# Performance work log

Measured on AMD Instinct MI355X. Metric: run time of the kernel, lower is better.

The kernel has to match this reference:

```python
import jax, jax.numpy as jnp
import numpy as np

N_E = 1024
E_DIM = 256
BETA = 0.25


def setup_inputs() -> dict:
    key = jax.random.key(0)
    k1, k2 = jax.random.split(key)
    z = jax.random.normal(k1, (16, 256, 64, 64), dtype=jnp.float32)
    # embedding initialized uniform(-1/n_e, 1/n_e)
    emb = jax.random.uniform(k2, (N_E, E_DIM), dtype=jnp.float32,
                             minval=-1.0 / N_E, maxval=1.0 / N_E)
    return {"z": z, "emb": emb}


def reference(z, emb):
    # z: [B, C, H, W] with C == e_dim; emb: [n_e, e_dim]
    z_perm = jnp.transpose(z, (0, 2, 3, 1))            # [B, H, W, C]
    zf = z_perm.reshape(-1, E_DIM)                      # [N, C]

    # pairwise squared distances: ||z||^2 + ||e||^2 - 2 z e^T  -> [N, n_e]
    d = (jnp.sum(zf * zf, axis=1, keepdims=True)
         + jnp.sum(emb * emb, axis=1)
         - 2.0 * jnp.matmul(zf, emb.T))

    idx = jnp.argmin(d, axis=1)                         # [N]
    zq_flat = emb[idx]                                  # gather [N, C]
    z_q = zq_flat.reshape(z_perm.shape)                 # [B, H, W, C]

    one_hot = jax.nn.one_hot(idx, N_E, dtype=jnp.float32)  # [N, n_e]

    codebook_loss = jnp.mean((jax.lax.stop_gradient(z_q) - z_perm) ** 2)
    commitment_loss = jnp.mean((z_q - jax.lax.stop_gradient(z_perm)) ** 2)
    loss = codebook_loss + BETA * commitment_loss

    # straight-through estimator
    z_q = z_perm + jax.lax.stop_gradient(z_q - z_perm)

    e_mean = jnp.mean(one_hot, axis=0)                  # [n_e]
    perplexity = jnp.exp(-jnp.sum(e_mean * jnp.log(e_mean + 1e-10)))

    z_q = jnp.transpose(z_q, (0, 3, 1, 2))              # [B, C, H, W]
    idx_ret = idx[:, None]
    return (z_q, loss, perplexity, one_hot, idx_ret, d)
```

## Files before the change

### kernel.cpp

```cpp
#include <hip/hip_runtime.h>
#include <math.h>


typedef unsigned short ushort;
typedef unsigned int uint;
typedef __attribute__((ext_vector_type(8))) short  bf16x8;
typedef __attribute__((ext_vector_type(8))) ushort ushort8v;
typedef __attribute__((ext_vector_type(4))) float  f32x4;

static const size_t O_LOSS = 16777216;
static const size_t O_PERP = 16777217;
static const size_t O_OH   = 16777218;
static const size_t O_IDX  = 83886082;
static const size_t O_D    = 83951618;

static const size_t WS_ENORM = 0;
static const size_t WS_ZNF   = 4096;
static const size_t WS_IDX   = 266240;
static const size_t WS_HIST  = 528384;
static const size_t WS_FCNT  = 532480;
static const size_t WS_FROWS = 532496;
static const size_t WS_LOSS  = 794640;
static const size_t WS_TOP2  = 802832;
static const size_t WS_AHI   = 9191440;
static const size_t WS_BHI   = 42745872;

#define THR_FLAG 4e-4f

__device__ __forceinline__ ushort f2bf(float f) {
  uint u = __float_as_uint(f);
  return (ushort)((u + 0x7FFFu + ((u >> 16) & 1u)) >> 16);
}
__device__ __forceinline__ void gload16(const void* g, void* l) {
  __builtin_amdgcn_global_load_lds(
      (const __attribute__((address_space(1))) void*)g,
      (__attribute__((address_space(3))) void*)l, 16, 0, 0);
}

__global__ __launch_bounds__(256) void vq_prep_e(const float* __restrict__ emb,
    float* __restrict__ enormf, ushort* __restrict__ Bhi,
    int* __restrict__ hist, int* __restrict__ flag_cnt) {
  const int j = blockIdx.x * 256 + threadIdx.x;
  hist[j] = 0;
  if (j == 0) *flag_cnt = 0;
  const float* e = emb + ((size_t)j << 8);
  ushort* br = Bhi + ((size_t)j << 8);
  double s = 0.0;
  for (int k0 = 0; k0 < 256; k0 += 8) {
    const float4 a = *(const float4*)&e[k0];
    const float4 b = *(const float4*)&e[k0 + 4];
    ushort8v v;
    v[0] = f2bf(a.x); v[1] = f2bf(a.y); v[2] = f2bf(a.z); v[3] = f2bf(a.w);
    v[4] = f2bf(b.x); v[5] = f2bf(b.y); v[6] = f2bf(b.z); v[7] = f2bf(b.w);
    *(ushort8v*)&br[k0] = v;
    s += (double)a.x * (double)a.x;  s += (double)a.y * (double)a.y;
    s += (double)a.z * (double)a.z;  s += (double)a.w * (double)a.w;
    s += (double)b.x * (double)b.x;  s += (double)b.y * (double)b.y;
    s += (double)b.z * (double)b.z;  s += (double)b.w * (double)b.w;
  }
  enormf[j] = (float)s;
}

__global__ __launch_bounds__(256) void vq_prep_z(const float* __restrict__ z,
    ushort* __restrict__ Ahi, float* __restrict__ znf) {
  __shared__ float As[256][68];
  __shared__ double znp[64][4];
  const int t = threadIdx.x;
  const int lane = t & 63, quad = t >> 6;
  const int blk = blockIdx.x;
  const float* zb = z + (((size_t)(blk >> 6)) << 20) + (((size_t)(blk & 63)) << 6);
  {
    const int kr = t >> 4, xc = (t & 15) << 2;
    for (int k0 = 0; k0 < 256; k0 += 16) {
      const int k = k0 + kr;
      *(float4*)&As[k][xc] = *(const float4*)&zb[((size_t)k << 12) + xc];
    }
  }
  __syncthreads();
  {
    double s = 0.0;
    const int kb = quad << 6;
    for (int k = 0; k < 64; ++k) { const double v = (double)As[kb + k][lane]; s += v * v; }
    znp[lane][quad] = s;
  }
  __syncthreads();
  const int m0 = ((blk >> 6) << 12) + ((blk & 63) << 6);
  if (t < 64) znf[m0 + t] = (float)(znp[t][0] + znp[t][1] + znp[t][2] + znp[t][3]);
  const int row = t >> 2;
  ushort* dst = Ahi + ((size_t)(m0 + row) << 8);
  for (int s = 0; s < 8; ++s) {
    const int k0 = ((t & 3) + (s << 2)) << 3;
    ushort8v v;
#pragma unroll
    for (int i = 0; i < 8; ++i) v[i] = f2bf(As[k0 + i][row]);
    *(ushort8v*)&dst[k0] = v;
  }
}

__global__ __launch_bounds__(256) void vq_gemm(const ushort* __restrict__ Ahi,
    const ushort* __restrict__ Bhi, const float* __restrict__ znf,
    const float* __restrict__ enormf, float* __restrict__ dmat,
    float4* __restrict__ top2) {
  __shared__ ushort As[16384];
  __shared__ ushort Bs[16384];

  const int t = threadIdx.x;
  const int lane = t & 63;
  const int w = t >> 6;
  const int wr = w >> 1, wc = w & 1;
  const int g = lane >> 4, cl = lane & 15;
  const int m0 = blockIdx.x << 7;
  const int n0 = blockIdx.y << 7;

  f32x4 acc[4][4];
#pragma unroll
  for (int a = 0; a < 4; ++a)
#pragma unroll
    for (int b = 0; b < 4; ++b) acc[a][b] = (f32x4)(0.0f);

  const int s0 = t, s1 = 256 + t;
  const int rA0 = s0 >> 2, cA0 = (s0 & 3) << 3;
  const int rA1 = s1 >> 2, cA1 = (s1 & 3) << 3;

#pragma unroll
  for (int p = 0; p < 2; ++p) {
    const int kb = p << 7;
    __syncthreads();
#pragma unroll
    for (int c = 0; c < 4; ++c) {
      const int koff = kb + (c << 5);
      gload16(Ahi + ((size_t)(m0 + rA0) << 8) + koff + cA0, &As[(c << 12) + (s0 << 3)]);
      gload16(Ahi + ((size_t)(m0 + rA1) << 8) + koff + cA1, &As[(c << 12) + (s1 << 3)]);
      gload16(Bhi + ((size_t)(n0 + rA0) << 8) + koff + cA0, &Bs[(c << 12) + (s0 << 3)]);
      gload16(Bhi + ((size_t)(n0 + rA1) << 8) + koff + cA1, &Bs[(c << 12) + (s1 << 3)]);
    }
    __syncthreads();
#pragma unroll
    for (int c2 = 0; c2 < 4; ++c2) {
      bf16x8 av[4], bv[4];
#pragma unroll
      for (int ai = 0; ai < 4; ++ai)
        av[ai] = *(const bf16x8*)&As[(c2 << 12) + ((wr << 6) + (ai << 4) + cl) * 32 + (g << 3)];
#pragma unroll
      for (int bj = 0; bj < 4; ++bj)
        bv[bj] = *(const bf16x8*)&Bs[(c2 << 12) + ((wc << 6) + (bj << 4) + cl) * 32 + (g << 3)];
#pragma unroll
      for (int ai = 0; ai < 4; ++ai)
#pragma unroll
        for (int bj = 0; bj < 4; ++bj)
          acc[ai][bj] = __builtin_amdgcn_mfma_f32_16x16x32_bf16(av[ai], bv[bj], acc[ai][bj], 0, 0, 0);
    }
  }

  __syncthreads();
  float* sd1 = (float*)As;
  int*   si1 = (int*)(sd1 + 256);
  float* sd2 = (float*)(si1 + 256);

  float zn_[4][4];
#pragma unroll
  for (int ai = 0; ai < 4; ++ai)
#pragma unroll
    for (int rg = 0; rg < 4; ++rg)
      zn_[ai][rg] = znf[m0 + (wr << 6) + (ai << 4) + (g << 2) + rg];
  float en_[4];
#pragma unroll
  for (int bj = 0; bj < 4; ++bj)
    en_[bj] = enormf[n0 + (wc << 6) + (bj << 4) + cl];

#pragma unroll
  for (int ai = 0; ai < 4; ++ai) {
#pragma unroll
    for (int rg = 0; rg < 4; ++rg) {
      const int m = m0 + (wr << 6) + (ai << 4) + (g << 2) + rg;
      const float zr = zn_[ai][rg];
      float m1 = 3.0e38f, m2 = 3.0e38f; int i1 = 0;
#pragma unroll
      for (int bj = 0; bj < 4; ++bj) {
        const float S = zr + en_[bj];
        const float v = S - 2.0f * acc[ai][bj][rg];
        const int n = n0 + (wc << 6) + (bj << 4) + cl;
        dmat[((size_t)m << 10) + n] = v;
        if (v < m1) { m2 = m1; m1 = v; i1 = n; }
        else if (v < m2) { m2 = v; }
      }
#pragma unroll
      for (int off = 8; off >= 1; off >>= 1) {
        const float o1 = __shfl_xor(m1, off, 16);
        const int   oi = __shfl_xor(i1, off, 16);
        const float o2 = __shfl_xor(m2, off, 16);
        const float ns = fminf(fminf(m2, o2), fmaxf(m1, o1));
        if (o1 < m1 || (o1 == m1 && oi < i1)) { m1 = o1; i1 = oi; }
        m2 = ns;
      }
      if (cl == 0) {
        const int r = (wr << 6) + (ai << 4) + (g << 2) + rg;
        sd1[(r << 1) + wc] = m1; si1[(r << 1) + wc] = i1; sd2[(r << 1) + wc] = m2;
      }
    }
  }
  __syncthreads();
  if (t < 128) {
    const float a1 = sd1[t << 1], b1 = sd1[(t << 1) + 1];
    const int ai1 = si1[t << 1], bi1 = si1[(t << 1) + 1];
    const float a2 = sd2[t << 1], b2 = sd2[(t << 1) + 1];
    float d1, d2; int i1;
    if (b1 < a1 || (b1 == a1 && bi1 < ai1)) { d1 = b1; i1 = bi1; d2 = fminf(a1, b2); }
    else { d1 = a1; i1 = ai1; d2 = fminf(b1, a2); }
    float4 r; r.x = d1; r.y = __int_as_float(i1); r.z = d2; r.w = 0.0f;
    top2[(((size_t)(m0 + t)) << 3) + blockIdx.y] = r;
  }
}

__global__ __launch_bounds__(256) void vq_top2merge(const float4* __restrict__ top2,
    int* __restrict__ idxw, int* __restrict__ flag_cnt, int* __restrict__ flag_rows,
    double* __restrict__ loss_part) {
  __shared__ double red[256];
  const int t = threadIdx.x;
  const int row = blockIdx.x * 256 + t;
  const float4* tp = top2 + ((size_t)row << 3);
  float4 e = tp[0];
  float d1 = e.x; int i1 = __float_as_int(e.y); float d2 = e.z;
  for (int k = 1; k < 8; ++k) {
    e = tp[k];
    const int ei = __float_as_int(e.y);
    if (e.x < d1 || (e.x == d1 && ei < i1)) { d2 = fminf(d1, e.z); d1 = e.x; i1 = ei; }
    else { d2 = fminf(d2, fminf(e.x, e.z)); }
  }
  idxw[row] = i1;
  if (d2 - d1 < THR_FLAG) {
    const int p = atomicAdd(flag_cnt, 1);
    flag_rows[p] = row;
  }
  red[t] = (double)d1;
  __syncthreads();
  for (int off = 128; off > 0; off >>= 1) {
    if (t < off) red[t] += red[t + off];
    __syncthreads();
  }
  if (t == 0) loss_part[blockIdx.x] = red[0];
}

__global__ __launch_bounds__(256) void vq_refine(const float* __restrict__ z,
    const float* __restrict__ emb, const float* __restrict__ znf,
    const float* __restrict__ enormf, const float* __restrict__ dmat,
    const int* __restrict__ flag_cnt, const int* __restrict__ flag_rows,
    int* __restrict__ idxw) {
  __shared__ float zrow[256];
  __shared__ float dmin_s[4];
  __shared__ int cand[256];
  __shared__ int ncand_s;
  __shared__ float rv[256];
  __shared__ int ri[256];
  const int t = threadIdx.x;
  const int n = *flag_cnt;
  for (int f = blockIdx.x; f < n; f += gridDim.x) {
    const int m = flag_rows[f];
    __syncthreads();
    if (t == 0) ncand_s = 0;
    zrow[t] = z[(((size_t)(m >> 12)) << 20) + (size_t)(m & 4095) + ((size_t)t << 12)];
    const float* dr = dmat + ((size_t)m << 10);
    const float2 a = *(const float2*)&dr[t << 2];
    const float2 b = *(const float2*)&dr[(t << 2) + 2];
    float dmin = fminf(fminf(a.x, a.y), fminf(b.x, b.y));
    for (int off = 32; off >= 1; off >>= 1) dmin = fminf(dmin, __shfl_xor(dmin, off));
    if ((t & 63) == 0) dmin_s[t >> 6] = dmin;
    __syncthreads();
    dmin = fminf(fminf(dmin_s[0], dmin_s[1]), fminf(dmin_s[2], dmin_s[3]));
    const float lim = dmin + THR_FLAG;
    const float dv[4] = {a.x, a.y, b.x, b.y};
#pragma unroll
    for (int q = 0; q < 4; ++q)
      if (dv[q] <= lim) {
        const int p = atomicAdd(&ncand_s, 1);
        if (p < 256) cand[p] = (t << 2) + q;
      }
    __syncthreads();
    const int nc = min(ncand_s, 256);
    float best = 3.0e38f; int bi = 1 << 30;
    if (t < nc) {
      const int j = cand[t];
      const float* er = emb + ((size_t)j << 8);
      float s = 0.0f;
      for (int k = 0; k < 256; ++k) s = fmaf(zrow[k], er[k], s);
      const float S = znf[m] + enormf[j];
      best = S - 2.0f * s;
      bi = j;
    }
    rv[t] = best; ri[t] = bi;
    __syncthreads();
    for (int off = 128; off > 0; off >>= 1) {
      if (t < off) {
        const float ov = rv[t + off]; const int oi = ri[t + off];
        if (ov < rv[t] || (ov == rv[t] && oi < ri[t])) { rv[t] = ov; ri[t] = oi; }
      }
      __syncthreads();
    }
    if (t == 0) idxw[m] = ri[0];
  }
}

__global__ __launch_bounds__(256) void vq_zq(const float* __restrict__ emb,
    const int* __restrict__ idxw, float* __restrict__ zq) {
  __shared__ float E[64][258];
  __shared__ int il[64];
  const int t = threadIdx.x;
  const int blk = blockIdx.x;
  const int base = blk << 6;
  if (t < 64) il[t] = idxw[base + t];
  __syncthreads();
  for (int i = 0; i < 64; ++i) E[i][t] = emb[((size_t)il[i] << 8) + t];
  __syncthreads();
  const int w = t & 63, cg = t >> 6;
  const size_t zbase = (((size_t)(blk >> 6)) << 20) + (((size_t)(blk & 63)) << 6) + (size_t)w;
  for (int ci = 0; ci < 64; ++ci) {
    const int c = (ci << 2) + cg;
    zq[zbase + ((size_t)c << 12)] = E[w][c];
  }
}

__global__ __launch_bounds__(256) void vq_scatter(const int* __restrict__ idxw,
    float* __restrict__ out, int* __restrict__ hist) {
  const int t = threadIdx.x;
  const int w = t >> 6, l = t & 63;
  const int rbase = (blockIdx.x << 6) + (w << 4);
  for (int rr = 0; rr < 16; ++rr) {
    const int m = rbase + rr;
    const int idx = idxw[m];
    float2* row = (float2*)(out + O_OH + ((size_t)m << 10));
    const int half = idx >> 1;
#pragma unroll
    for (int i = 0; i < 8; ++i) {
      const int slot = (i << 6) + l;
      float2 v; v.x = 0.0f; v.y = 0.0f;
      if (slot == half) { if (idx & 1) v.y = 1.0f; else v.x = 1.0f; }
      row[slot] = v;
    }
    if (l == 0) {
      out[O_IDX + m] = (float)idx;
      atomicAdd(&hist[idx], 1);
    }
  }
}

__global__ __launch_bounds__(256) void vq_final(const double* __restrict__ loss_part,
    const int* __restrict__ hist, float* __restrict__ out) {
  __shared__ double red[256];
  const int t = threadIdx.x;
  red[t] = loss_part[t];
  __syncthreads();
  for (int off = 128; off > 0; off >>= 1) {
    if (t < off) red[t] += red[t + off];
    __syncthreads();
  }
  if (t == 0) out[O_LOSS] = (float)(1.25 * red[0] / 16777216.0);
  __syncthreads();
  double h = 0.0;
  for (int i = t; i < 1024; i += 256) {
    const double p = (double)hist[i] / 65536.0;
    h += p * log(p + 1e-10);
  }
  red[t] = h;
  __syncthreads();
  for (int off = 128; off > 0; off >>= 1) {
    if (t < off) red[t] += red[t + off];
    __syncthreads();
  }
  if (t == 0) out[O_PERP] = (float)exp(-red[0]);
}

extern "C" void kernel_launch(void* const* d_in, const int* in_sizes, int n_in,
                              void* d_out, int out_size, void* d_ws, size_t ws_size,
                              hipStream_t stream) {
  const float* z   = (const float*)d_in[0];
  const float* emb = (const float*)d_in[1];
  float* out = (float*)d_out;
  char* ws = (char*)d_ws;

  float*  enormf    = (float*)(ws + WS_ENORM);
  float*  znf       = (float*)(ws + WS_ZNF);
  int*    idxw      = (int*)(ws + WS_IDX);
  int*    hist      = (int*)(ws + WS_HIST);
  int*    flag_cnt  = (int*)(ws + WS_FCNT);
  int*    flag_rows = (int*)(ws + WS_FROWS);
  double* loss_part = (double*)(ws + WS_LOSS);
  float4* top2      = (float4*)(ws + WS_TOP2);
  ushort* Ahi       = (ushort*)(ws + WS_AHI);
  ushort* Bhi       = (ushort*)(ws + WS_BHI);

  vq_prep_e<<<4, 256, 0, stream>>>(emb, enormf, Bhi, hist, flag_cnt);
  vq_prep_z<<<1024, 256, 0, stream>>>(z, Ahi, znf);
  dim3 g(512, 8);
  vq_gemm<<<g, 256, 0, stream>>>(Ahi, Bhi, znf, enormf, out + O_D, top2);
  vq_top2merge<<<256, 256, 0, stream>>>(top2, idxw, flag_cnt, flag_rows, loss_part);
  vq_refine<<<4096, 256, 0, stream>>>(z, emb, znf, enormf, out + O_D,
                                      flag_cnt, flag_rows, idxw);
  vq_zq<<<1024, 256, 0, stream>>>(emb, idxw, out);
  vq_scatter<<<1024, 256, 0, stream>>>(idxw, out, hist);
  vq_final<<<1, 256, 0, stream>>>(loss_part, hist, out);
}
```

Before: 387.3 us.

## Fuse GEMM, top-2 merge and one-hot scatter into one persistent-row kernel

Replaces the 2D-tiled GEMM with a kernel where each 512-thread block owns 128 rows of z and keeps them resident in LDS (XOR-swizzled layout written by prep_z), streaming the codebook through a double-buffered B tile. Running top-2 minima are kept in registers across all 1024 codes, which removes the top2 workspace round trip and the separate merge and scatter kernels. The same kernel writes idx, the histogram and the one-hot rows. The refine kernel now patches the one-hot, idx and histogram only for rows whose argmin changes. The costs are re-reading the full codebook per block, a __syncthreads every k-chunk, and less parallelism per block.

```diff
diff --git a/kernel.cpp b/kernel.cpp
--- a/kernel.cpp
+++ b/kernel.cpp
@@ -21,7 +21,6 @@
 static const size_t WS_FCNT  = 532480;
 static const size_t WS_FROWS = 532496;
 static const size_t WS_LOSS  = 794640;
-static const size_t WS_TOP2  = 802832;
 static const size_t WS_AHI   = 9191440;
 static const size_t WS_BHI   = 42745872;
 
@@ -87,116 +86,137 @@
   const int m0 = ((blk >> 6) << 12) + ((blk & 63) << 6);
   if (t < 64) znf[m0 + t] = (float)(znp[t][0] + znp[t][1] + znp[t][2] + znp[t][3]);
   const int row = t >> 2;
+  const int swz = (row & 7) << 3;
   ushort* dst = Ahi + ((size_t)(m0 + row) << 8);
   for (int s = 0; s < 8; ++s) {
     const int k0 = ((t & 3) + (s << 2)) << 3;
     ushort8v v;
 #pragma unroll
     for (int i = 0; i < 8; ++i) v[i] = f2bf(As[k0 + i][row]);
-    *(ushort8v*)&dst[k0] = v;
-  }
-}
-
-__global__ __launch_bounds__(256) void vq_gemm(const ushort* __restrict__ Ahi,
+    *(ushort8v*)&dst[k0 ^ swz] = v;
+  }
+}
+
+__global__ __launch_bounds__(512, 4) void vq_mega(const ushort* __restrict__ Ahi,
     const ushort* __restrict__ Bhi, const float* __restrict__ znf,
-    const float* __restrict__ enormf, float* __restrict__ dmat,
-    float4* __restrict__ top2) {
-  __shared__ ushort As[16384];
-  __shared__ ushort Bs[16384];
+    const float* __restrict__ enormf, float* __restrict__ out,
+    int* __restrict__ idxw, int* __restrict__ hist,
+    int* __restrict__ flag_cnt, int* __restrict__ flag_rows,
+    double* __restrict__ loss_part) {
+  __shared__ ushort As[32768];
+  __shared__ ushort Bs[2][4096];
 
   const int t = threadIdx.x;
   const int lane = t & 63;
   const int w = t >> 6;
-  const int wr = w >> 1, wc = w & 1;
+  const int wr = w >> 1;
+  const int wc = w & 1;
   const int g = lane >> 4, cl = lane & 15;
   const int m0 = blockIdx.x << 7;
-  const int n0 = blockIdx.y << 7;
-
-  f32x4 acc[4][4];
-#pragma unroll
-  for (int a = 0; a < 4; ++a)
+  float* dmat = out + O_D;
+
+  {
+    const size_t abase = (size_t)m0 << 8;
+    const int off = t << 3;
+#pragma unroll
+    for (int i = 0; i < 8; ++i)
+      gload16(Ahi + abase + (i << 12) + off, &As[(i << 12) + off]);
+    gload16(Bhi + ((size_t)(t >> 2) << 8) + ((t & 3) << 3), &Bs[0][t << 3]);
+  }
+
+  float zn_[2][4];
+#pragma unroll
+  for (int ai = 0; ai < 2; ++ai)
+#pragma unroll
+    for (int rg = 0; rg < 4; ++rg)
+      zn_[ai][rg] = znf[m0 + (wr << 5) + (ai << 4) + (g << 2) + rg];
+
+  f32x4 acc[2][4];
+#pragma unroll
+  for (int a = 0; a < 2; ++a)
 #pragma unroll
     for (int b = 0; b < 4; ++b) acc[a][b] = (f32x4)(0.0f);
-
-  const int s0 = t, s1 = 256 + t;
-  const int rA0 = s0 >> 2, cA0 = (s0 & 3) << 3;
-  const int rA1 = s1 >> 2, cA1 = (s1 & 3) << 3;
-
-#pragma unroll
-  for (int p = 0; p < 2; ++p) {
-    const int kb = p << 7;
-    __syncthreads();
-#pragma unroll
-    for (int c = 0; c < 4; ++c) {
-      const int koff = kb + (c << 5);
-      gload16(Ahi + ((size_t)(m0 + rA0) << 8) + koff + cA0, &As[(c << 12) + (s0 << 3)]);
-      gload16(Ahi + ((size_t)(m0 + rA1) << 8) + koff + cA1, &As[(c << 12) + (s1 << 3)]);
-      gload16(Bhi + ((size_t)(n0 + rA0) << 8) + koff + cA0, &Bs[(c << 12) + (s0 << 3)]);
-      gload16(Bhi + ((size_t)(n0 + rA1) << 8) + koff + cA1, &Bs[(c << 12) + (s1 << 3)]);
-    }
-    __syncthreads();
-#pragma unroll
-    for (int c2 = 0; c2 < 4; ++c2) {
-      bf16x8 av[4], bv[4];
-#pragma unroll
-      for (int ai = 0; ai < 4; ++ai)
-        av[ai] = *(const bf16x8*)&As[(c2 << 12) + ((wr << 6) + (ai << 4) + cl) * 32 + (g << 3)];
+  float run1[8], run2[8]; int runi[8];
+#pragma unroll
+  for (int r = 0; r < 8; ++r) { run1[r] = 3.0e38f; run2[r] = 3.0e38f; runi[r] = 0; }
+
+  __syncthreads();
+
+  int cur = 0;
+  for (int it = 0; it < 64; ++it) {
+    const int nt = it >> 3, kch = it & 7;
+    if (it < 63) {
+      const int nit = it + 1;
+      const int nnt = nit >> 3, nkch = nit & 7;
+      gload16(Bhi + ((size_t)(nnt) << 15) + (nkch << 5) +
+                  ((size_t)(t >> 2) << 8) + ((t & 3) << 3),
+              &Bs[cur ^ 1][t << 3]);
+    }
+    {
+      const int kb = kch << 5;
+      bf16x8 av[2], bv[4];
+#pragma unroll
+      for (int ai = 0; ai < 2; ++ai) {
+        const int row = (wr << 5) + (ai << 4) + cl;
+        av[ai] = *(const bf16x8*)&As[(row << 8) + ((kb + (g << 3)) ^ ((cl & 7) << 3))];
+      }
 #pragma unroll
       for (int bj = 0; bj < 4; ++bj)
-        bv[bj] = *(const bf16x8*)&Bs[(c2 << 12) + ((wc << 6) + (bj << 4) + cl) * 32 + (g << 3)];
-#pragma unroll
-      for (int ai = 0; ai < 4; ++ai)
+        bv[bj] = *(const bf16x8*)&Bs[cur][(((wc << 6) + (bj << 4) + cl) << 5) + (g << 3)];
+#pragma unroll
+      for (int ai = 0; ai < 2; ++ai)
 #pragma unroll
         for (int bj = 0; bj < 4; ++bj)
           acc[ai][bj] = __builtin_amdgcn_mfma_f32_16x16x32_bf16(av[ai], bv[bj], acc[ai][bj], 0, 0, 0);
     }
-  }
-
-  __syncthreads();
-  float* sd1 = (float*)As;
-  int*   si1 = (int*)(sd1 + 256);
-  float* sd2 = (float*)(si1 + 256);
-
-  float zn_[4][4];
-#pragma unroll
-  for (int ai = 0; ai < 4; ++ai)
-#pragma unroll
-    for (int rg = 0; rg < 4; ++rg)
-      zn_[ai][rg] = znf[m0 + (wr << 6) + (ai << 4) + (g << 2) + rg];
-  float en_[4];
-#pragma unroll
-  for (int bj = 0; bj < 4; ++bj)
-    en_[bj] = enormf[n0 + (wc << 6) + (bj << 4) + cl];
-
-#pragma unroll
-  for (int ai = 0; ai < 4; ++ai) {
-#pragma unroll
-    for (int rg = 0; rg < 4; ++rg) {
-      const int m = m0 + (wr << 6) + (ai << 4) + (g << 2) + rg;
-      const float zr = zn_[ai][rg];
-      float m1 = 3.0e38f, m2 = 3.0e38f; int i1 = 0;
-#pragma unroll
-      for (int bj = 0; bj < 4; ++bj) {
-        const float S = zr + en_[bj];
-        const float v = S - 2.0f * acc[ai][bj][rg];
-        const int n = n0 + (wc << 6) + (bj << 4) + cl;
-        dmat[((size_t)m << 10) + n] = v;
-        if (v < m1) { m2 = m1; m1 = v; i1 = n; }
-        else if (v < m2) { m2 = v; }
+    if (kch == 7) {
+      float en_[4];
+#pragma unroll
+      for (int bj = 0; bj < 4; ++bj)
+        en_[bj] = enormf[(nt << 7) + (wc << 6) + (bj << 4) + cl];
+#pragma unroll
+      for (int ai = 0; ai < 2; ++ai) {
+#pragma unroll
+        for (int bj = 0; bj < 4; ++bj) {
+          const int n = (nt << 7) + (wc << 6) + (bj << 4) + cl;
+#pragma unroll
+          for (int rg = 0; rg < 4; ++rg) {
+            const float S = zn_[ai][rg] + en_[bj];
+            const float v = S - 2.0f * acc[ai][bj][rg];
+            const int m = m0 + (wr << 5) + (ai << 4) + (g << 2) + rg;
+            dmat[((size_t)m << 10) + n] = v;
+            const int rr = (ai << 2) + rg;
+            if (v < run1[rr]) { run2[rr] = run1[rr]; run1[rr] = v; runi[rr] = n; }
+            else if (v < run2[rr]) { run2[rr] = v; }
+          }
+          acc[ai][bj] = (f32x4)(0.0f);
+        }
       }
-#pragma unroll
-      for (int off = 8; off >= 1; off >>= 1) {
-        const float o1 = __shfl_xor(m1, off, 16);
-        const int   oi = __shfl_xor(i1, off, 16);
-        const float o2 = __shfl_xor(m2, off, 16);
-        const float ns = fminf(fminf(m2, o2), fmaxf(m1, o1));
-        if (o1 < m1 || (o1 == m1 && oi < i1)) { m1 = o1; i1 = oi; }
-        m2 = ns;
-      }
-      if (cl == 0) {
-        const int r = (wr << 6) + (ai << 4) + (g << 2) + rg;
-        sd1[(r << 1) + wc] = m1; si1[(r << 1) + wc] = i1; sd2[(r << 1) + wc] = m2;
-      }
+    }
+    __syncthreads();
+    cur ^= 1;
+  }
+
+  float*  sd1  = (float*)As;
+  int*    si1  = (int*)((char*)As + 1024);
+  float*  sd2  = (float*)((char*)As + 2048);
+  int*    idxs = (int*)((char*)As + 3072);
+  double* red  = (double*)((char*)As + 3584);
+
+#pragma unroll
+  for (int rr = 0; rr < 8; ++rr) {
+    float a1 = run1[rr], a2 = run2[rr]; int ai1 = runi[rr];
+    for (int off = 8; off >= 1; off >>= 1) {
+      const float o1 = __shfl_xor(a1, off, 16);
+      const int   oi = __shfl_xor(ai1, off, 16);
+      const float o2 = __shfl_xor(a2, off, 16);
+      const float ns = fminf(fminf(a2, o2), fmaxf(a1, o1));
+      if (o1 < a1 || (o1 == a1 && oi < ai1)) { a1 = o1; ai1 = oi; }
+      a2 = ns;
+    }
+    if (cl == 0) {
+      const int r = (wr << 5) + ((rr >> 2) << 4) + (g << 2) + (rr & 3);
+      sd1[(r << 1) + wc] = a1; si1[(r << 1) + wc] = ai1; sd2[(r << 1) + wc] = a2;
     }
   }
   __syncthreads();
@@ -207,51 +227,52 @@
     float d1, d2; int i1;
     if (b1 < a1 || (b1 == a1 && bi1 < ai1)) { d1 = b1; i1 = bi1; d2 = fminf(a1, b2); }
     else { d1 = a1; i1 = ai1; d2 = fminf(b1, a2); }
-    float4 r; r.x = d1; r.y = __int_as_float(i1); r.z = d2; r.w = 0.0f;
-    top2[(((size_t)(m0 + t)) << 3) + blockIdx.y] = r;
-  }
-}
-
-__global__ __launch_bounds__(256) void vq_top2merge(const float4* __restrict__ top2,
-    int* __restrict__ idxw, int* __restrict__ flag_cnt, int* __restrict__ flag_rows,
-    double* __restrict__ loss_part) {
-  __shared__ double red[256];
-  const int t = threadIdx.x;
-  const int row = blockIdx.x * 256 + t;
-  const float4* tp = top2 + ((size_t)row << 3);
-  float4 e = tp[0];
-  float d1 = e.x; int i1 = __float_as_int(e.y); float d2 = e.z;
-  for (int k = 1; k < 8; ++k) {
-    e = tp[k];
-    const int ei = __float_as_int(e.y);
-    if (e.x < d1 || (e.x == d1 && ei < i1)) { d2 = fminf(d1, e.z); d1 = e.x; i1 = ei; }
-    else { d2 = fminf(d2, fminf(e.x, e.z)); }
-  }
-  idxw[row] = i1;
-  if (d2 - d1 < THR_FLAG) {
-    const int p = atomicAdd(flag_cnt, 1);
-    flag_rows[p] = row;
-  }
-  red[t] = (double)d1;
-  __syncthreads();
-  for (int off = 128; off > 0; off >>= 1) {
+    const int m = m0 + t;
+    idxw[m] = i1; idxs[t] = i1;
+    out[O_IDX + m] = (float)i1;
+    atomicAdd(&hist[i1], 1);
+    if (d2 - d1 < THR_FLAG) {
+      const int p = atomicAdd(flag_cnt, 1);
+      flag_rows[p] = m;
+    }
+    red[t] = (double)d1;
+  }
+  __syncthreads();
+  for (int off = 64; off > 0; off >>= 1) {
     if (t < off) red[t] += red[t + off];
     __syncthreads();
   }
   if (t == 0) loss_part[blockIdx.x] = red[0];
+  __syncthreads();
+
+  float2* ohbase = (float2*)(out + O_OH);
+  for (int rr = 0; rr < 16; ++rr) {
+    const int r = (w << 4) + rr;
+    const int idx = idxs[r];
+    float2* row = ohbase + (((size_t)(m0 + r)) << 9);
+    const int half = idx >> 1;
+#pragma unroll
+    for (int i = 0; i < 8; ++i) {
+      const int slot = (i << 6) + lane;
+      float2 v; v.x = 0.0f; v.y = 0.0f;
+      if (slot == half) { if (idx & 1) v.y = 1.0f; else v.x = 1.0f; }
+      row[slot] = v;
+    }
+  }
 }
 
 __global__ __launch_bounds__(256) void vq_refine(const float* __restrict__ z,
     const float* __restrict__ emb, const float* __restrict__ znf,
-    const float* __restrict__ enormf, const float* __restrict__ dmat,
-    const int* __restrict__ flag_cnt, const int* __restrict__ flag_rows,
-    int* __restrict__ idxw) {
+    const float* __restrict__ enormf, const int* __restrict__ flag_cnt,
+    const int* __restrict__ flag_rows, int* __restrict__ idxw,
+    float* __restrict__ out, int* __restrict__ hist) {
   __shared__ float zrow[256];
   __shared__ float dmin_s[4];
   __shared__ int cand[256];
   __shared__ int ncand_s;
   __shared__ float rv[256];
   __shared__ int ri[256];
+  const float* dmat = out + O_D;
   const int t = threadIdx.x;
   const int n = *flag_cnt;
   for (int f = blockIdx.x; f < n; f += gridDim.x) {
@@ -296,7 +317,18 @@
       }
       __syncthreads();
     }
-    if (t == 0) idxw[m] = ri[0];
+    if (t == 0) {
+      const int nbi = ri[0];
+      const int old = idxw[m];
+      if (nbi != old) {
+        idxw[m] = nbi;
+        out[O_IDX + m] = (float)nbi;
+        out[O_OH + ((size_t)m << 10) + (size_t)old] = 0.0f;
+        out[O_OH + ((size_t)m << 10) + (size_t)nbi] = 1.0f;
+        atomicAdd(&hist[old], -1);
+        atomicAdd(&hist[nbi], 1);
+      }
+    }
   }
 }
 
@@ -319,35 +351,11 @@
   }
 }
 
-__global__ __launch_bounds__(256) void vq_scatter(const int* __restrict__ idxw,
-    float* __restrict__ out, int* __restrict__ hist) {
-  const int t = threadIdx.x;
-  const int w = t >> 6, l = t & 63;
-  const int rbase = (blockIdx.x << 6) + (w << 4);
-  for (int rr = 0; rr < 16; ++rr) {
-    const int m = rbase + rr;
-    const int idx = idxw[m];
-    float2* row = (float2*)(out + O_OH + ((size_t)m << 10));
-    const int half = idx >> 1;
-#pragma unroll
-    for (int i = 0; i < 8; ++i) {
-      const int slot = (i << 6) + l;
-      float2 v; v.x = 0.0f; v.y = 0.0f;
-      if (slot == half) { if (idx & 1) v.y = 1.0f; else v.x = 1.0f; }
-      row[slot] = v;
-    }
-    if (l == 0) {
-      out[O_IDX + m] = (float)idx;
-      atomicAdd(&hist[idx], 1);
-    }
-  }
-}
-
 __global__ __launch_bounds__(256) void vq_final(const double* __restrict__ loss_part,
     const int* __restrict__ hist, float* __restrict__ out) {
   __shared__ double red[256];
   const int t = threadIdx.x;
-  red[t] = loss_part[t];
+  red[t] = loss_part[t] + loss_part[t + 256];
   __syncthreads();
   for (int off = 128; off > 0; off >>= 1) {
     if (t < off) red[t] += red[t + off];
@@ -384,18 +392,15 @@
   int*    flag_cnt  = (int*)(ws + WS_FCNT);
   int*    flag_rows = (int*)(ws + WS_FROWS);
   double* loss_part = (double*)(ws + WS_LOSS);
-  float4* top2      = (float4*)(ws + WS_TOP2);
   ushort* Ahi       = (ushort*)(ws + WS_AHI);
   ushort* Bhi       = (ushort*)(ws + WS_BHI);
 
   vq_prep_e<<<4, 256, 0, stream>>>(emb, enormf, Bhi, hist, flag_cnt);
   vq_prep_z<<<1024, 256, 0, stream>>>(z, Ahi, znf);
-  dim3 g(512, 8);
-  vq_gemm<<<g, 256, 0, stream>>>(Ahi, Bhi, znf, enormf, out + O_D, top2);
-  vq_top2merge<<<256, 256, 0, stream>>>(top2, idxw, flag_cnt, flag_rows, loss_part);
-  vq_refine<<<4096, 256, 0, stream>>>(z, emb, znf, enormf, out + O_D,
-                                      flag_cnt, flag_rows, idxw);
+  vq_mega<<<512, 512, 0, stream>>>(Ahi, Bhi, znf, enormf, out, idxw, hist,
+                                   flag_cnt, flag_rows, loss_part);
+  vq_refine<<<4096, 256, 0, stream>>>(z, emb, znf, enormf, flag_cnt, flag_rows,
+                                      idxw, out, hist);
   vq_zq<<<1024, 256, 0, stream>>>(emb, idxw, out);
-  vq_scatter<<<1024, 256, 0, stream>>>(idxw, out, hist);
   vq_final<<<1, 256, 0, stream>>>(loss_part, hist, out);
 }
```

Result: faster. 326.6 us (-15.7%).
